# Kernel tuning notes

Hardware: AMD Instinct MI355X
Metric: run time of the kernel (lower is better)

Reference implementation:

```python
import jax, jax.numpy as jnp
import numpy as np

D_MODEL = 256
N_HEADS = 8
N_LEVELS = 4
N_POINTS = 4
DH = D_MODEL // N_HEADS
SHAPES = [(100, 150), (50, 75), (25, 38), (13, 19)]  # per-level (H, W)
BATCH = 2


def setup_inputs() -> dict:
    key = jax.random.key(0)
    ks = jax.random.split(key, 8)
    Lq = sum(h * w for h, w in SHAPES)  # 19947
    d = D_MODEL
    off_dim = N_HEADS * N_LEVELS * N_POINTS * 2
    aw_dim = N_HEADS * N_LEVELS * N_POINTS
    s = 1.0 / np.sqrt(d).astype(np.float32)
    lsi = np.concatenate([[0], np.cumsum([h * w for h, w in SHAPES])[:-1]])
    return {
        "query": jax.random.normal(ks[0], (BATCH, Lq, d), jnp.float32),
        "reference_points": jax.random.uniform(ks[1], (BATCH, Lq, N_LEVELS, 2), jnp.float32),
        "input_flatten": jax.random.normal(ks[2], (BATCH, Lq, d), jnp.float32),
        "input_spatial_shapes": jnp.array(SHAPES, dtype=jnp.int32),
        "input_level_start_index": jnp.array(lsi, dtype=jnp.int32),
        "W_samp": 0.01 * jax.random.normal(ks[3], (off_dim, d), jnp.float32),
        "b_samp": 0.1 * jax.random.normal(ks[4], (off_dim,), jnp.float32),
        "W_attn": s * jax.random.normal(ks[5], (aw_dim, d), jnp.float32),
        "b_attn": jnp.zeros((aw_dim,), jnp.float32),
        "W_val": s * jax.random.normal(ks[6], (d, d), jnp.float32),
        "b_val": jnp.zeros((d,), jnp.float32),
        "W_out": s * jax.random.normal(ks[7], (d, d), jnp.float32),
        "b_out": jnp.zeros((d,), jnp.float32),
    }


def _bilinear(v, grid, Hl, Wl):
    # v: [N, H, Hl*Wl, Dh] flattened level feature map per head
    # grid: [N, H, Q, P, 2] in [-1, 1]; align_corners=False, zero padding
    N, H, Q, P, _ = grid.shape
    Dh = v.shape[-1]
    x = (grid[..., 0] + 1.0) * 0.5 * Wl - 0.5
    y = (grid[..., 1] + 1.0) * 0.5 * Hl - 0.5
    x0 = jnp.floor(x)
    y0 = jnp.floor(y)
    lx = x - x0
    ly = y - y0
    x0i = x0.astype(jnp.int32)
    y0i = y0.astype(jnp.int32)

    def corner(xi, yi, w):
        valid = (xi >= 0) & (xi < Wl) & (yi >= 0) & (yi < Hl)
        idx = jnp.clip(yi, 0, Hl - 1) * Wl + jnp.clip(xi, 0, Wl - 1)
        g = jnp.take_along_axis(v, idx.reshape(N, H, Q * P, 1), axis=2)
        return g.reshape(N, H, Q, P, Dh) * (w * valid)[..., None]

    return (corner(x0i, y0i, (1 - lx) * (1 - ly))
            + corner(x0i + 1, y0i, lx * (1 - ly))
            + corner(x0i, y0i + 1, (1 - lx) * ly)
            + corner(x0i + 1, y0i + 1, lx * ly))


def _forward(query, ref, x, shapes, W_samp, b_samp, W_attn, b_attn, W_val, b_val, W_out, b_out):
    N, Lq, d = query.shape
    H, L, P, Dh = N_HEADS, N_LEVELS, N_POINTS, DH
    # value projection -> [N, H, S, Dh]
    value = (x @ W_val.T + b_val).reshape(N, -1, H, Dh).transpose(0, 2, 1, 3)
    off = (query @ W_samp.T + b_samp).reshape(N, Lq, H, L, P, 2)
    attw = jax.nn.softmax((query @ W_attn.T + b_attn).reshape(N, Lq, H, L * P), axis=-1)
    attw = attw.reshape(N, Lq, H, L, P).transpose(0, 2, 1, 3, 4)  # [N,H,Lq,L,P]
    # offset normalizer is (W, H) per level
    norm = jnp.array([[w, h] for h, w in shapes], dtype=query.dtype)  # [L, 2]
    loc = ref[:, :, None, :, None, :] + off / norm[None, None, None, :, None, :]
    grids = (2.0 * loc - 1.0).transpose(0, 2, 1, 3, 4, 5)  # [N,H,Lq,L,P,2]

    acc = jnp.zeros((N, Lq, H, Dh), query.dtype)
    start = 0
    for lvl, (Hl, Wl) in enumerate(shapes):
        v = value[:, :, start:start + Hl * Wl]  # [N,H,Hl*Wl,Dh]
        start += Hl * Wl
        samp = _bilinear(v, grids[:, :, :, lvl], Hl, Wl)  # [N,H,Lq,P,Dh]
        acc = acc + jnp.einsum('nhqpd,nhqp->nqhd', samp, attw[:, :, :, lvl])
    out = acc.reshape(N, Lq, H * Dh)
    return out @ W_out.T + b_out


def reference(query, reference_points, input_flatten, input_spatial_shapes,
              input_level_start_index, W_samp, b_samp, W_attn, b_attn,
              W_val, b_val, W_out, b_out):
    shapes = [(int(h), int(w)) for h, w in np.asarray(input_spatial_shapes)]
    return _forward(query, reference_points, input_flatten, shapes,
                    W_samp, b_samp, W_attn, b_attn, W_val, b_val, W_out, b_out)
```

## Files before the change

### kernel.cpp

```cpp
#include <hip/hip_runtime.h>
#include <hip/hip_bf16.h>

#define NB 2
#define LQ 19947
#define LV 19947
#define DM 256
#define NH 8
#define NL 4
#define NP 4
#define MROWS (NB*LQ)
#define MPAD  39936
#define QPB 2

__device__ __constant__ int c_lvlH[4] = {100, 50, 25, 13};
__device__ __constant__ int c_lvlW[4] = {150, 75, 38, 19};
__device__ __constant__ int c_lvlS[4] = {0, 15000, 18750, 19700};

typedef __attribute__((ext_vector_type(8))) short short8;
typedef __attribute__((ext_vector_type(4))) float f32x4;
typedef __attribute__((ext_vector_type(2))) float f32x2;

__device__ __forceinline__ unsigned short f2bf(float f) {
  unsigned u = __float_as_uint(f);
  u += 0x7FFFu + ((u >> 16) & 1u);
  return (unsigned short)(u >> 16);
}
__device__ __forceinline__ float bfl(unsigned u) { return __uint_as_float(u << 16); }
__device__ __forceinline__ float bfh(unsigned u) { return __uint_as_float(u & 0xFFFF0000u); }
__device__ __forceinline__ f32x2 up2(unsigned u) {
  f32x2 r; r.x = __uint_as_float(u << 16); r.y = __uint_as_float(u & 0xFFFF0000u); return r;
}
__device__ __forceinline__ unsigned cvtpk(float lo, float hi) {
  unsigned r;
  asm("v_cvt_pk_bf16_f32 %0, %1, %2" : "=v"(r) : "v"(lo), "v"(hi));
  return r;
}

__global__ __launch_bounds__(256) void gemm_front(
    const float* __restrict__ xin, const float* __restrict__ query,
    const float* __restrict__ Wv, const float* __restrict__ Wsamp,
    const float* __restrict__ Wattn,
    const float* __restrict__ b_val, const float* __restrict__ b_samp,
    const float* __restrict__ b_attn,
    unsigned short* __restrict__ value, unsigned short* __restrict__ oc)
{
  const float* Af; const float* Bf; const float* biasp;
  unsigned short* Cp; int Nn, cb, bro;
  if (blockIdx.y < 2) {
    Af = xin; Bf = Wv; cb = blockIdx.y; bro = cb * 128;
    biasp = b_val + cb * 128; Cp = value; Nn = 256;
  } else {
    Af = query; cb = blockIdx.y - 2; Cp = oc; Nn = 384;
    if (cb < 2) { Bf = Wsamp; bro = cb * 128; biasp = b_samp + cb * 128; }
    else        { Bf = Wattn; bro = 0;        biasp = b_attn; }
  }

  __shared__ alignas(16) short As[2][128 * 32];
  __shared__ alignas(16) short Bs[2][128 * 32];

  const int t = threadIdx.x;
  const int w = t >> 6, l = t & 63;
  const int wr = w >> 1, wc = w & 1;
  const size_t rowBase = (size_t)blockIdx.x * 128;
  const int colBase = cb * 128;

  const f32x4 z = {0.f, 0.f, 0.f, 0.f};
  f32x4 acc[4][4];
  #pragma unroll
  for (int i = 0; i < 4; ++i)
    #pragma unroll
    for (int j = 0; j < 4; ++j) acc[i][j] = z;

  const int srow = t >> 1;
  const int skh  = (t & 1) * 16;
  const int swz  = (srow & 6) << 2;
  const int sc0  = skh ^ swz;
  const int sc1  = (skh + 8) ^ swz;
  const int arow_ok = ((int)rowBase + srow) < MROWS;
  const float* apBase = Af + ((size_t)rowBase + srow) * 256 + skh;
  const float* bpBase = Bf + (size_t)(bro + srow) * 256 + skh;
  const float4 fz4 = make_float4(0.f, 0.f, 0.f, 0.f);

  float4 a0, a1, a2, a3, b0, b1, b2, b3;
#define LOADA(K) do { if (arow_ok) { const float* ap = apBase + (K); \
    a0 = *(const float4*)ap; a1 = *(const float4*)(ap + 4); \
    a2 = *(const float4*)(ap + 8); a3 = *(const float4*)(ap + 12); } \
    else { a0 = fz4; a1 = fz4; a2 = fz4; a3 = fz4; } } while (0)
#define LOADB(K) do { const float* bp = bpBase + (K); \
    b0 = *(const float4*)bp; b1 = *(const float4*)(bp + 4); \
    b2 = *(const float4*)(bp + 8); b3 = *(const float4*)(bp + 12); } while (0)
#define STAGE(BUF) do { \
    uint4 wA0, wA1, wB0, wB1; \
    wA0.x = cvtpk(a0.x, a0.y); wA0.y = cvtpk(a0.z, a0.w); \
    wA0.z = cvtpk(a1.x, a1.y); wA0.w = cvtpk(a1.z, a1.w); \
    wA1.x = cvtpk(a2.x, a2.y); wA1.y = cvtpk(a2.z, a2.w); \
    wA1.z = cvtpk(a3.x, a3.y); wA1.w = cvtpk(a3.z, a3.w); \
    wB0.x = cvtpk(b0.x, b0.y); wB0.y = cvtpk(b0.z, b0.w); \
    wB0.z = cvtpk(b1.x, b1.y); wB0.w = cvtpk(b1.z, b1.w); \
    wB1.x = cvtpk(b2.x, b2.y); wB1.y = cvtpk(b2.z, b2.w); \
    wB1.z = cvtpk(b3.x, b3.y); wB1.w = cvtpk(b3.z, b3.w); \
    *(uint4*)&As[BUF][srow * 32 + sc0] = wA0; \
    *(uint4*)&As[BUF][srow * 32 + sc1] = wA1; \
    *(uint4*)&Bs[BUF][srow * 32 + sc0] = wB0; \
    *(uint4*)&Bs[BUF][srow * 32 + sc1] = wB1; } while (0)

  LOADA(0); LOADB(0);
  STAGE(0);
  LOADA(32); LOADB(32);
  __syncthreads();

  for (int ks = 0; ks < 8; ++ks) {
    const int cur = ks & 1;
    if (ks < 7) STAGE(cur ^ 1);
    if (ks < 6) { LOADA((ks + 2) * 32); LOADB((ks + 2) * 32); }
    short8 af[4], bf[4];
    #pragma unroll
    for (int i = 0; i < 4; ++i) {
      const int ar = wr * 64 + i * 16 + (l & 15);
      const int br = wc * 64 + i * 16 + (l & 15);
      const int cs = (l >> 4) * 8;
      af[i] = *(const short8*)&As[cur][ar * 32 + (cs ^ ((ar & 6) << 2))];
      bf[i] = *(const short8*)&Bs[cur][br * 32 + (cs ^ ((br & 6) << 2))];
    }
    #pragma unroll
    for (int i = 0; i < 4; ++i)
      #pragma unroll
      for (int j = 0; j < 4; ++j)
        acc[i][j] = __builtin_amdgcn_mfma_f32_16x16x32_bf16(bf[j], af[i], acc[i][j], 0, 0, 0);
    __syncthreads();
  }
#undef LOADA
#undef LOADB
#undef STAGE

  const int row0 = (int)rowBase + wr * 64 + (l & 15);
  const int lc0 = wc * 64 + (l >> 4) * 4;
  const int col0 = colBase + lc0;
  #pragma unroll
  for (int j = 0; j < 4; ++j) {
    const float4 bj = *(const float4*)(biasp + lc0 + j * 16);
    #pragma unroll
    for (int i = 0; i < 4; ++i) {
      const int row = row0 + i * 16;
      uint2 st;
      st.x = (unsigned)f2bf(acc[i][j][0] + bj.x) | ((unsigned)f2bf(acc[i][j][1] + bj.y) << 16);
      st.y = (unsigned)f2bf(acc[i][j][2] + bj.z) | ((unsigned)f2bf(acc[i][j][3] + bj.w) << 16);
      *(uint2*)(Cp + (size_t)row * Nn + col0 + j * 16) = st;
    }
  }
}

__global__ __launch_bounds__(256) void gemm_out(
    const unsigned short* __restrict__ Ab, const float* __restrict__ Wof,
    const float* __restrict__ bias, float* __restrict__ Cp)
{
  __shared__ alignas(16) short As[2][128 * 32];
  __shared__ alignas(16) short Bs[2][128 * 32];

  const int t = threadIdx.x;
  const int w = t >> 6, l = t & 63;
  const int wr = w >> 1, wc = w & 1;
  const size_t rowBase = (size_t)blockIdx.x * 128;
  const int colBase = blockIdx.y * 128;

  const f32x4 z = {0.f, 0.f, 0.f, 0.f};
  f32x4 acc[4][4];
  #pragma unroll
  for (int i = 0; i < 4; ++i)
    #pragma unroll
    for (int j = 0; j < 4; ++j) acc[i][j] = z;

  const int srow = t >> 1;
  const int skh  = (t & 1) * 16;
  const int swz  = (srow & 6) << 2;
  const int sc0  = skh ^ swz;
  const int sc1  = (skh + 8) ^ swz;
  const unsigned short* apBase = Ab + ((size_t)rowBase + srow) * 256 + skh;
  const float* bpBase = Wof + (size_t)(colBase + srow) * 256 + skh;

  uint4 av0, av1;
  float4 b0, b1, b2, b3;
#define LOADA(K) do { const unsigned short* ap = apBase + (K); \
    av0 = *(const uint4*)ap; av1 = *(const uint4*)(ap + 8); } while (0)
#define LOADB(K) do { const float* bp = bpBase + (K); \
    b0 = *(const float4*)bp; b1 = *(const float4*)(bp + 4); \
    b2 = *(const float4*)(bp + 8); b3 = *(const float4*)(bp + 12); } while (0)
#define STAGE(BUF) do { \
    uint4 wB0, wB1; \
    wB0.x = cvtpk(b0.x, b0.y); wB0.y = cvtpk(b0.z, b0.w); \
    wB0.z = cvtpk(b1.x, b1.y); wB0.w = cvtpk(b1.z, b1.w); \
    wB1.x = cvtpk(b2.x, b2.y); wB1.y = cvtpk(b2.z, b2.w); \
    wB1.z = cvtpk(b3.x, b3.y); wB1.w = cvtpk(b3.z, b3.w); \
    *(uint4*)&As[BUF][srow * 32 + sc0] = av0; \
    *(uint4*)&As[BUF][srow * 32 + sc1] = av1; \
    *(uint4*)&Bs[BUF][srow * 32 + sc0] = wB0; \
    *(uint4*)&Bs[BUF][srow * 32 + sc1] = wB1; } while (0)

  LOADA(0); LOADB(0);
  STAGE(0);
  LOADA(32); LOADB(32);
  __syncthreads();

  for (int ks = 0; ks < 8; ++ks) {
    const int cur = ks & 1;
    if (ks < 7) STAGE(cur ^ 1);
    if (ks < 6) { LOADA((ks + 2) * 32); LOADB((ks + 2) * 32); }
    short8 af[4], bf[4];
    #pragma unroll
    for (int i = 0; i < 4; ++i) {
      const int ar = wr * 64 + i * 16 + (l & 15);
      const int br = wc * 64 + i * 16 + (l & 15);
      const int cs = (l >> 4) * 8;
      af[i] = *(const short8*)&As[cur][ar * 32 + (cs ^ ((ar & 6) << 2))];
      bf[i] = *(const short8*)&Bs[cur][br * 32 + (cs ^ ((br & 6) << 2))];
    }
    #pragma unroll
    for (int i = 0; i < 4; ++i)
      #pragma unroll
      for (int j = 0; j < 4; ++j)
        acc[i][j] = __builtin_amdgcn_mfma_f32_16x16x32_bf16(bf[j], af[i], acc[i][j], 0, 0, 0);
    __syncthreads();
  }
#undef LOADA
#undef LOADB
#undef STAGE

  const int row0 = (int)rowBase + wr * 64 + (l & 15);
  const int col0 = colBase + wc * 64 + (l >> 4) * 4;
  #pragma unroll
  for (int j = 0; j < 4; ++j) {
    const float4 bj = *(const float4*)(bias + col0 + j * 16);
    #pragma unroll
    for (int i = 0; i < 4; ++i) {
      const int row = row0 + i * 16;
      if (row < MROWS) {
        *(float4*)(Cp + (size_t)row * 256 + col0 + j * 16) =
            make_float4(acc[i][j][0] + bj.x, acc[i][j][1] + bj.y,
                        acc[i][j][2] + bj.z, acc[i][j][3] + bj.w);
      }
    }
  }
}

__global__ __launch_bounds__(128) void msda_sample(
    const unsigned short* __restrict__ value,
    const float* __restrict__ refp,
    const unsigned short* __restrict__ oc,
    unsigned short* __restrict__ accb)
{
  __shared__ float s_aw[QPB][128];
  __shared__ float s_ref[QPB][8];
  __shared__ alignas(16) unsigned s_pk[QPB][NH][17][8];

  const int t = threadIdx.x;
  const int bq0 = blockIdx.x * QPB;

  {
    const int q = t >> 6, i = t & 63;
    const int bq = bq0 + q;
    const unsigned pw = *(const unsigned*)(oc + (size_t)bq * 384 + 256 + i * 2);
    s_aw[q][i * 2 + 0] = bfl(pw);
    s_aw[q][i * 2 + 1] = bfh(pw);
    if (t < QPB * 8) {
      const int q2 = t >> 3, j = t & 7;
      s_ref[q2][j] = refp[(size_t)(bq0 + q2) * 8 + j];
    }
  }
  __syncthreads();

  if (t < QPB * NH) {
    const int q = t >> 3, h = t & 7;
    float* aw = &s_aw[q][h * 16];
    float m = aw[0];
    #pragma unroll
    for (int i = 1; i < 16; ++i) m = fmaxf(m, aw[i]);
    float e[16]; float s = 0.f;
    #pragma unroll
    for (int i = 0; i < 16; ++i) { e[i] = __expf(aw[i] - m); s += e[i]; }
    const float inv = 1.f / s;
    #pragma unroll
    for (int i = 0; i < 16; ++i) aw[i] = e[i] * inv;
  }
  __syncthreads();

  #pragma unroll
  for (int it = t; it < QPB * 128; it += 128) {
    const int q = it >> 7, rem = it & 127;
    const int h = rem >> 4, idx = rem & 15;
    const int l = idx >> 2;
    const int bq = bq0 + q;
    const unsigned po = *(const unsigned*)(oc + (size_t)bq * 384 + rem * 2);
    const int Hl = c_lvlH[l], Wl = c_lvlW[l], st = c_lvlS[l];
    const float x = s_ref[q][l * 2 + 0] * (float)Wl - 0.5f + bfl(po);
    const float y = s_ref[q][l * 2 + 1] * (float)Hl - 0.5f + bfh(po);
    const float aw = s_aw[q][rem];
    const float x0f = floorf(x), y0f = floorf(y);
    const float lx = x - x0f, ly = y - y0f;
    const int x0 = (int)x0f, y0 = (int)y0f;
    const float vx0 = (x0 >= 0 && x0 < Wl) ? 1.f : 0.f;
    const float vx1 = (x0 >= -1 && x0 < Wl - 1) ? 1.f : 0.f;
    const float vy0 = (y0 >= 0 && y0 < Hl) ? 1.f : 0.f;
    const float vy1 = (y0 >= -1 && y0 < Hl - 1) ? 1.f : 0.f;
    const int xc0 = min(max(x0, 0), Wl - 1);
    const int xc1 = min(max(x0 + 1, 0), Wl - 1);
    const int yc0 = min(max(y0, 0), Hl - 1);
    const int yc1 = min(max(y0 + 1, 0), Hl - 1);
    const int r0 = st + yc0 * Wl, r1 = st + yc1 * Wl;
    uint4 g0, g1;
    g0.x = (unsigned)(r0 + xc0) * 512u;
    g0.y = (unsigned)(r0 + xc1) * 512u;
    g0.z = __float_as_uint((1.f - lx) * (1.f - ly) * aw * (vx0 * vy0));
    g0.w = __float_as_uint(lx * (1.f - ly) * aw * (vx1 * vy0));
    g1.x = (unsigned)(r1 + xc0) * 512u;
    g1.y = (unsigned)(r1 + xc1) * 512u;
    g1.z = __float_as_uint((1.f - lx) * ly * aw * (vx0 * vy1));
    g1.w = __float_as_uint(lx * ly * aw * (vx1 * vy1));
    *(uint4*)&s_pk[q][h][idx][0] = g0;
    *(uint4*)&s_pk[q][h][idx][4] = g1;
  }
  __syncthreads();

  const int wv = t >> 6;
  const int lane = t & 63;
  const int bq = bq0 + wv;
  const int n = bq / LQ;
  const char* vbase = (const char*)value + (size_t)n * LV * 512;
  const int h = lane >> 3;
  const int c2 = (lane >> 2) & 1;
  const unsigned laneoff = (unsigned)(h * 64 + (lane & 3) * 16);

  f32x2 acc0 = {0.f, 0.f}, acc1 = {0.f, 0.f}, acc2 = {0.f, 0.f}, acc3 = {0.f, 0.f};

#define PKRD(i) (*(const uint4*)&s_pk[wv][h][(i)][c2 * 4])
#define GLD(o)  (*(const uint4*)(vbase + (o) + laneoff))

  uint4 pk0 = PKRD(0), pk1 = PKRD(1), pk2 = PKRD(2), pk3 = PKRD(3);
  uint4 va0 = GLD(pk0.x), vb0 = GLD(pk0.y);
  uint4 va1 = GLD(pk1.x), vb1 = GLD(pk1.y);
  uint4 va2 = GLD(pk2.x), vb2 = GLD(pk2.y);

  #pragma unroll
  for (int idx = 0; idx < 16; ++idx) {
    uint4 va3, vb3, pk4;
    if (idx < 13) { va3 = GLD(pk3.x); vb3 = GLD(pk3.y); }
    if (idx < 12) { pk4 = PKRD(idx + 4); }
    const float was = __uint_as_float(pk0.z);
    const float wbs = __uint_as_float(pk0.w);
    f32x2 wa; wa.x = was; wa.y = was;
    f32x2 wb; wb.x = wbs; wb.y = wbs;
    acc0 = acc0 + wa * up2(va0.x);
    acc1 = acc1 + wa * up2(va0.y);
    acc2 = acc2 + wa * up2(va0.z);
    acc3 = acc3 + wa * up2(va0.w);
    acc0 = acc0 + wb * up2(vb0.x);
    acc1 = acc1 + wb * up2(vb0.y);
    acc2 = acc2 + wb * up2(vb0.z);
    acc3 = acc3 + wb * up2(vb0.w);
    pk0 = pk1; pk1 = pk2; pk2 = pk3; pk3 = pk4;
    va0 = va1; va1 = va2; va2 = va3;
    vb0 = vb1; vb1 = vb2; vb2 = vb3;
  }
#undef PKRD
#undef GLD

  acc0.x += __shfl_xor(acc0.x, 4); acc0.y += __shfl_xor(acc0.y, 4);
  acc1.x += __shfl_xor(acc1.x, 4); acc1.y += __shfl_xor(acc1.y, 4);
  acc2.x += __shfl_xor(acc2.x, 4); acc2.y += __shfl_xor(acc2.y, 4);
  acc3.x += __shfl_xor(acc3.x, 4); acc3.y += __shfl_xor(acc3.y, 4);

  if (c2 == 0) {
    uint4 st;
    st.x = (unsigned)f2bf(acc0.x) | ((unsigned)f2bf(acc0.y) << 16);
    st.y = (unsigned)f2bf(acc1.x) | ((unsigned)f2bf(acc1.y) << 16);
    st.z = (unsigned)f2bf(acc2.x) | ((unsigned)f2bf(acc2.y) << 16);
    st.w = (unsigned)f2bf(acc3.x) | ((unsigned)f2bf(acc3.y) << 16);
    *(uint4*)((char*)accb + (size_t)bq * 512 + laneoff) = st;
  }
}

extern "C" void kernel_launch(void* const* d_in, const int* in_sizes, int n_in,
                              void* d_out, int out_size, void* d_ws, size_t ws_size,
                              hipStream_t stream) {
  const float* query  = (const float*)d_in[0];
  const float* refp   = (const float*)d_in[1];
  const float* xin    = (const float*)d_in[2];
  const float* W_samp = (const float*)d_in[5];
  const float* b_samp = (const float*)d_in[6];
  const float* W_attn = (const float*)d_in[7];
  const float* b_attn = (const float*)d_in[8];
  const float* W_val  = (const float*)d_in[9];
  const float* b_val  = (const float*)d_in[10];
  const float* W_out  = (const float*)d_in[11];
  const float* b_out  = (const float*)d_in[12];
  float* out = (float*)d_out;
  (void)in_sizes; (void)n_in; (void)out_size; (void)ws_size;

  char* ws = (char*)d_ws;
  unsigned short* value = (unsigned short*)(ws);
  unsigned short* accb  = (unsigned short*)(ws + 20447232);
  unsigned short* oc    = (unsigned short*)(ws + 40894464);

  hipLaunchKernelGGL(gemm_front, dim3(312, 5), dim3(256), 0, stream,
                     xin, query, W_val, W_samp, W_attn, b_val, b_samp, b_attn,
                     value, oc);
  hipLaunchKernelGGL(msda_sample, dim3(MROWS / QPB), dim3(128), 0, stream,
                     value, refp, oc, accb);
  hipLaunchKernelGGL(gemm_out, dim3(312, 2), dim3(256), 0, stream,
                     accb, W_out, b_out, out);
}
```

Before: 250.9 us.

## Deepen GEMM global prefetch, request two blocks per CU, repad sampler LDS

Both GEMM kernels now keep a deeper register prefetch pipeline: A loads are issued three k-steps ahead and B loads two ahead, using rotating register buffers, and the k-loop is fully unrolled. Launch bounds request two blocks per CU to keep occupancy under the added register pressure. In the sampler, the per-head sample pack table gets a padded stride of 140 words instead of 136 to reduce LDS bank conflicts. The deeper prefetch costs more registers, which could cause spills or force the occupancy hint to limit unrolling.

```diff
diff --git a/kernel.cpp b/kernel.cpp
--- a/kernel.cpp
+++ b/kernel.cpp
@@ -36,7 +36,7 @@
   return r;
 }
 
-__global__ __launch_bounds__(256) void gemm_front(
+__global__ __launch_bounds__(256, 2) void gemm_front(
     const float* __restrict__ xin, const float* __restrict__ query,
     const float* __restrict__ Wv, const float* __restrict__ Wsamp,
     const float* __restrict__ Wattn,
@@ -81,38 +81,35 @@
   const float* bpBase = Bf + (size_t)(bro + srow) * 256 + skh;
   const float4 fz4 = make_float4(0.f, 0.f, 0.f, 0.f);
 
-  float4 a0, a1, a2, a3, b0, b1, b2, b3;
-#define LOADA(K) do { if (arow_ok) { const float* ap = apBase + (K); \
-    a0 = *(const float4*)ap; a1 = *(const float4*)(ap + 4); \
-    a2 = *(const float4*)(ap + 8); a3 = *(const float4*)(ap + 12); } \
-    else { a0 = fz4; a1 = fz4; a2 = fz4; a3 = fz4; } } while (0)
-#define LOADB(K) do { const float* bp = bpBase + (K); \
-    b0 = *(const float4*)bp; b1 = *(const float4*)(bp + 4); \
-    b2 = *(const float4*)(bp + 8); b3 = *(const float4*)(bp + 12); } while (0)
-#define STAGE(BUF) do { \
-    uint4 wA0, wA1, wB0, wB1; \
-    wA0.x = cvtpk(a0.x, a0.y); wA0.y = cvtpk(a0.z, a0.w); \
-    wA0.z = cvtpk(a1.x, a1.y); wA0.w = cvtpk(a1.z, a1.w); \
-    wA1.x = cvtpk(a2.x, a2.y); wA1.y = cvtpk(a2.z, a2.w); \
-    wA1.z = cvtpk(a3.x, a3.y); wA1.w = cvtpk(a3.z, a3.w); \
-    wB0.x = cvtpk(b0.x, b0.y); wB0.y = cvtpk(b0.z, b0.w); \
-    wB0.z = cvtpk(b1.x, b1.y); wB0.w = cvtpk(b1.z, b1.w); \
-    wB1.x = cvtpk(b2.x, b2.y); wB1.y = cvtpk(b2.z, b2.w); \
-    wB1.z = cvtpk(b3.x, b3.y); wB1.w = cvtpk(b3.z, b3.w); \
-    *(uint4*)&As[BUF][srow * 32 + sc0] = wA0; \
-    *(uint4*)&As[BUF][srow * 32 + sc1] = wA1; \
-    *(uint4*)&Bs[BUF][srow * 32 + sc0] = wB0; \
-    *(uint4*)&Bs[BUF][srow * 32 + sc1] = wB1; } while (0)
-
-  LOADA(0); LOADB(0);
-  STAGE(0);
-  LOADA(32); LOADB(32);
+  float4 a[3][4];
+  float4 b[2][4];
+
+#define LD16(dst, base, K) do { const float* p_ = (base) + (K) * 32; \
+    dst[0] = *(const float4*)p_;       dst[1] = *(const float4*)(p_ + 4); \
+    dst[2] = *(const float4*)(p_ + 8); dst[3] = *(const float4*)(p_ + 12); } while (0)
+#define LDAZ(dst, K) do { if (arow_ok) { LD16(dst, apBase, K); } \
+    else { dst[0] = fz4; dst[1] = fz4; dst[2] = fz4; dst[3] = fz4; } } while (0)
+#define ST16(ARR, BUF, src) do { uint4 w0_, w1_; \
+    w0_.x = cvtpk(src[0].x, src[0].y); w0_.y = cvtpk(src[0].z, src[0].w); \
+    w0_.z = cvtpk(src[1].x, src[1].y); w0_.w = cvtpk(src[1].z, src[1].w); \
+    w1_.x = cvtpk(src[2].x, src[2].y); w1_.y = cvtpk(src[2].z, src[2].w); \
+    w1_.z = cvtpk(src[3].x, src[3].y); w1_.w = cvtpk(src[3].z, src[3].w); \
+    *(uint4*)&ARR[BUF][srow * 32 + sc0] = w0_; \
+    *(uint4*)&ARR[BUF][srow * 32 + sc1] = w1_; } while (0)
+
+  LDAZ(a[0], 0); LD16(b[0], bpBase, 0);
+  LDAZ(a[1], 1); LD16(b[1], bpBase, 1);
+  LDAZ(a[2], 2);
+  ST16(As, 0, a[0]); ST16(Bs, 0, b[0]);
+  LDAZ(a[0], 3); LD16(b[0], bpBase, 2);
   __syncthreads();
 
+  #pragma unroll
   for (int ks = 0; ks < 8; ++ks) {
     const int cur = ks & 1;
-    if (ks < 7) STAGE(cur ^ 1);
-    if (ks < 6) { LOADA((ks + 2) * 32); LOADB((ks + 2) * 32); }
+    if (ks < 7) { ST16(As, cur ^ 1, a[(ks + 1) % 3]); ST16(Bs, cur ^ 1, b[(ks + 1) & 1]); }
+    if (ks + 4 < 8) LDAZ(a[(ks + 1) % 3], ks + 4);
+    if (ks + 3 < 8) LD16(b[(ks + 1) & 1], bpBase, ks + 3);
     short8 af[4], bf[4];
     #pragma unroll
     for (int i = 0; i < 4; ++i) {
@@ -129,9 +126,9 @@
         acc[i][j] = __builtin_amdgcn_mfma_f32_16x16x32_bf16(bf[j], af[i], acc[i][j], 0, 0, 0);
     __syncthreads();
   }
-#undef LOADA
-#undef LOADB
-#undef STAGE
+#undef LD16
+#undef LDAZ
+#undef ST16
 
   const int row0 = (int)rowBase + wr * 64 + (l & 15);
   const int lc0 = wc * 64 + (l >> 4) * 4;
@@ -150,7 +147,7 @@
   }
 }
 
-__global__ __launch_bounds__(256) void gemm_out(
+__global__ __launch_bounds__(256, 2) void gemm_out(
     const unsigned short* __restrict__ Ab, const float* __restrict__ Wof,
     const float* __restrict__ bias, float* __restrict__ Cp)
 {
@@ -178,33 +175,38 @@
   const unsigned short* apBase = Ab + ((size_t)rowBase + srow) * 256 + skh;
   const float* bpBase = Wof + (size_t)(colBase + srow) * 256 + skh;
 
-  uint4 av0, av1;
-  float4 b0, b1, b2, b3;
-#define LOADA(K) do { const unsigned short* ap = apBase + (K); \
-    av0 = *(const uint4*)ap; av1 = *(const uint4*)(ap + 8); } while (0)
-#define LOADB(K) do { const float* bp = bpBase + (K); \
-    b0 = *(const float4*)bp; b1 = *(const float4*)(bp + 4); \
-    b2 = *(const float4*)(bp + 8); b3 = *(const float4*)(bp + 12); } while (0)
-#define STAGE(BUF) do { \
-    uint4 wB0, wB1; \
-    wB0.x = cvtpk(b0.x, b0.y); wB0.y = cvtpk(b0.z, b0.w); \
-    wB0.z = cvtpk(b1.x, b1.y); wB0.w = cvtpk(b1.z, b1.w); \
-    wB1.x = cvtpk(b2.x, b2.y); wB1.y = cvtpk(b2.z, b2.w); \
-    wB1.z = cvtpk(b3.x, b3.y); wB1.w = cvtpk(b3.z, b3.w); \
-    *(uint4*)&As[BUF][srow * 32 + sc0] = av0; \
-    *(uint4*)&As[BUF][srow * 32 + sc1] = av1; \
-    *(uint4*)&Bs[BUF][srow * 32 + sc0] = wB0; \
-    *(uint4*)&Bs[BUF][srow * 32 + sc1] = wB1; } while (0)
-
-  LOADA(0); LOADB(0);
-  STAGE(0);
-  LOADA(32); LOADB(32);
+  uint4 av[3][2];
+  float4 b[2][4];
+
+#define LDA2(dst, K) do { const unsigned short* p_ = apBase + (K) * 32; \
+    dst[0] = *(const uint4*)p_; dst[1] = *(const uint4*)(p_ + 8); } while (0)
+#define LD16(dst, K) do { const float* p_ = bpBase + (K) * 32; \
+    dst[0] = *(const float4*)p_;       dst[1] = *(const float4*)(p_ + 4); \
+    dst[2] = *(const float4*)(p_ + 8); dst[3] = *(const float4*)(p_ + 12); } while (0)
+#define STA(BUF, src) do { \
+    *(uint4*)&As[BUF][srow * 32 + sc0] = src[0]; \
+    *(uint4*)&As[BUF][srow * 32 + sc1] = src[1]; } while (0)
+#define STB(BUF, src) do { uint4 w0_, w1_; \
+    w0_.x = cvtpk(src[0].x, src[0].y); w0_.y = cvtpk(src[0].z, src[0].w); \
+    w0_.z = cvtpk(src[1].x, src[1].y); w0_.w = cvtpk(src[1].z, src[1].w); \
+    w1_.x = cvtpk(src[2].x, src[2].y); w1_.y = cvtpk(src[2].z, src[2].w); \
+    w1_.z = cvtpk(src[3].x, src[3].y); w1_.w = cvtpk(src[3].z, src[3].w); \
+    *(uint4*)&Bs[BUF][srow * 32 + sc0] = w0_; \
+    *(uint4*)&Bs[BUF][srow * 32 + sc1] = w1_; } while (0)
+
+  LDA2(av[0], 0); LD16(b[0], 0);
+  LDA2(av[1], 1); LD16(b[1], 1);
+  LDA2(av[2], 2);
+  STA(0, av[0]); STB(0, b[0]);
+  LDA2(av[0], 3); LD16(b[0], 2);
   __syncthreads();
 
+  #pragma unroll
   for (int ks = 0; ks < 8; ++ks) {
     const int cur = ks & 1;
-    if (ks < 7) STAGE(cur ^ 1);
-    if (ks < 6) { LOADA((ks + 2) * 32); LOADB((ks + 2) * 32); }
+    if (ks < 7) { STA(cur ^ 1, av[(ks + 1) % 3]); STB(cur ^ 1, b[(ks + 1) & 1]); }
+    if (ks + 4 < 8) LDA2(av[(ks + 1) % 3], ks + 4);
+    if (ks + 3 < 8) LD16(b[(ks + 1) & 1], ks + 3);
     short8 af[4], bf[4];
     #pragma unroll
     for (int i = 0; i < 4; ++i) {
@@ -221,9 +223,10 @@
         acc[i][j] = __builtin_amdgcn_mfma_f32_16x16x32_bf16(bf[j], af[i], acc[i][j], 0, 0, 0);
     __syncthreads();
   }
-#undef LOADA
-#undef LOADB
-#undef STAGE
+#undef LDA2
+#undef LD16
+#undef STA
+#undef STB
 
   const int row0 = (int)rowBase + wr * 64 + (l & 15);
   const int col0 = colBase + wc * 64 + (l >> 4) * 4;
@@ -250,7 +253,7 @@
 {
   __shared__ float s_aw[QPB][128];
   __shared__ float s_ref[QPB][8];
-  __shared__ alignas(16) unsigned s_pk[QPB][NH][17][8];
+  __shared__ alignas(16) unsigned s_pku[2240];
 
   const int t = threadIdx.x;
   const int bq0 = blockIdx.x * QPB;
@@ -315,8 +318,9 @@
     g1.y = (unsigned)(r1 + xc1) * 512u;
     g1.z = __float_as_uint((1.f - lx) * ly * aw * (vx0 * vy1));
     g1.w = __float_as_uint(lx * ly * aw * (vx1 * vy1));
-    *(uint4*)&s_pk[q][h][idx][0] = g0;
-    *(uint4*)&s_pk[q][h][idx][4] = g1;
+    unsigned* wp_ = &s_pku[q * 1120 + h * 140 + idx * 8];
+    *(uint4*)wp_ = g0;
+    *(uint4*)(wp_ + 4) = g1;
   }
   __syncthreads();
 
@@ -331,7 +335,7 @@
 
   f32x2 acc0 = {0.f, 0.f}, acc1 = {0.f, 0.f}, acc2 = {0.f, 0.f}, acc3 = {0.f, 0.f};
 
-#define PKRD(i) (*(const uint4*)&s_pk[wv][h][(i)][c2 * 4])
+#define PKRD(i) (*(const uint4*)&s_pku[wv * 1120 + h * 140 + (i) * 8 + c2 * 4])
 #define GLD(o)  (*(const uint4*)(vbase + (o) + laneoff))
 
   uint4 pk0 = PKRD(0), pk1 = PKRD(1), pk2 = PKRD(2), pk3 = PKRD(3);
```

After: 265.6 us. 5.9% more time.
